# Kernel tuning notes

Measured on AMD Instinct MI355X. Metric: run time of the kernel, lower is better.

Reference implementation:

```python
import jax, jax.numpy as jnp
import numpy as np

N = 100000          # nodes
E = 1600000         # edges (avg degree 16)
F_IN = 128          # node_feature_dim
D = 64              # state_dim
LATENT = 32         # latent_dim -> output 2*latent
ROUNDS = 4


def setup_inputs() -> dict:
    key = jax.random.key(0)
    ks = jax.random.split(key, 12)
    s = 0.05  # weight scale
    return {
        "x": jax.random.normal(ks[0], (N, F_IN), dtype=jnp.float32),
        "edge_index": jax.random.randint(ks[1], (2, E), 0, N, dtype=jnp.int64),
        "batch": jnp.zeros((N,), dtype=jnp.int64),
        # input MLP: Linear(F_IN, D) + ReLU + Linear(D, D) + ReLU
        "W1": jax.random.normal(ks[2], (F_IN, D), dtype=jnp.float32) * s,
        "b1": jnp.zeros((D,), dtype=jnp.float32),
        "W2": jax.random.normal(ks[3], (D, D), dtype=jnp.float32) * s,
        "b2": jnp.zeros((D,), dtype=jnp.float32),
        # per-round GraphConv params (PyG: lin_rel has bias, lin_root does not)
        "Wrel": jax.random.normal(ks[4], (ROUNDS, D, D), dtype=jnp.float32) * s,
        "brel": jnp.zeros((ROUNDS, D), dtype=jnp.float32),
        "Wroot": jax.random.normal(ks[5], (ROUNDS, D, D), dtype=jnp.float32) * s,
        # output Linear(D, 2*latent)
        "Wout": jax.random.normal(ks[6], (D, 2 * LATENT), dtype=jnp.float32) * s,
        "bout": jnp.zeros((2 * LATENT,), dtype=jnp.float32),
    }


def reference(x, edge_index, batch, W1, b1, W2, b2, Wrel, brel, Wroot, Wout, bout):
    # input MLP (ends with ReLU) followed by the extra F.relu in forward (idempotent, kept for fidelity)
    h = jax.nn.relu(x @ W1 + b1)
    h = jax.nn.relu(h @ W2 + b2)
    h = jax.nn.relu(h)
    src, dst = edge_index[0], edge_index[1]
    n = h.shape[0]
    num_rounds = Wrel.shape[0]
    for r in range(num_rounds):
        # GraphConv: scatter-add of source features to destinations, then lin_rel + lin_root
        agg = jax.ops.segment_sum(h[src], dst, num_segments=n)  # [N, D]
        conv = agg @ Wrel[r] + brel[r] + h @ Wroot[r]
        h = h + jax.nn.relu(conv)  # residual
    return h @ Wout + bout  # [N, 2*latent]
```

## Files before the change

### kernel.cpp

```cpp
#include <hip/hip_runtime.h>
#include <hip/hip_bf16.h>

#define CAP 48
#define NPASS 4
#define WP 72
#define WP1 136

typedef __attribute__((ext_vector_type(8))) _Float16 f16x8;
typedef __attribute__((ext_vector_type(4))) float f32x4;

__global__ void k_init(int4* __restrict__ deg4, _Float16* __restrict__ hh,
                       int ndeg4, int n)
{
    const int i = blockIdx.x * 256 + threadIdx.x;
    const int4 z = {0, 0, 0, 0};
    for (int j = i; j < ndeg4; j += gridDim.x * 256) deg4[j] = z;
    if (blockIdx.x == 0 && threadIdx.x < 64)
        hh[(size_t)n * 64 + threadIdx.x] = (_Float16)0.f;
}

__global__ void k_fillp(const int* __restrict__ ei, int* __restrict__ deg,
                        int* __restrict__ colp, int E, int lo, int hi)
{
    int e = blockIdx.x * 256 + threadIdx.x;
    if (e < E) {
        int dst = ei[E + e];
        if (dst >= lo && dst < hi) {
            int pos = atomicAdd(&deg[dst], 1);
            if (pos < CAP) colp[(size_t)dst * CAP + pos] = ei[e];
        }
    }
}

__global__ void k_pad(const int* __restrict__ deg, int* __restrict__ colp, int n)
{
    const int i = blockIdx.x * 256 + threadIdx.x;
    const int node = i >> 4, s = i & 15;
    if (node < n) {
        const int cnt = min(deg[node], CAP);
        const int end = (cnt + 15) & ~15;
        const int slot = cnt + s;
        if (slot < end) colp[(size_t)node * CAP + slot] = n;
    }
}

__global__ __launch_bounds__(256) void k_gather(
    const _Float16* __restrict__ hh, _Float16* __restrict__ aggh,
    const int* __restrict__ colp, const int* __restrict__ deg, int n)
{
    const int w = threadIdx.x >> 6, lane = threadIdx.x & 63;
    const int r = lane >> 3, c = lane & 7;
    const int node = blockIdx.x * 4 + w;
    if (node >= n) return;
    const int cnt = min(deg[node], CAP);

    const int* cb = &colp[(size_t)node * CAP];
    f16x8 s0 = {}; f16x8 s1 = {};
    for (int jb = 0; jb < cnt; jb += 16) {
        const int2 cq = *(const int2*)&cb[jb + 2 * r];
        s0 += *(const f16x8*)&hh[(size_t)cq.x * 64 + c * 8];
        s1 += *(const f16x8*)&hh[(size_t)cq.y * 64 + c * 8];
    }
    s0 += s1;
    #pragma unroll
    for (int st = 8; st <= 32; st <<= 1) {
        uint4 u = *(uint4*)&s0, t;
        t.x = __shfl_xor(u.x, st);
        t.y = __shfl_xor(u.y, st);
        t.z = __shfl_xor(u.z, st);
        t.w = __shfl_xor(u.w, st);
        s0 += *(f16x8*)&t;
    }
    if (r == 0)
        *(uint4*)&aggh[(size_t)node * 64 + c * 8] = *(uint4*)&s0;
}


__global__ __launch_bounds__(256) void k_mlp_mfma(
    const float* __restrict__ x,
    const float* __restrict__ W1, const float* __restrict__ b1,
    const float* __restrict__ W2, const float* __restrict__ b2,
    _Float16* __restrict__ hh, int n)
{
    __shared__ _Float16 W1T[64 * WP1];
    __shared__ _Float16 W2T[64 * WP];
    __shared__ _Float16 t1[4][16 * WP];
    __shared__ float b1s[64], b2s[64];

    const int tid = threadIdx.x;
    for (int i = tid; i < 128 * 64; i += 256) {
        const int k = i >> 6, c = i & 63;
        W1T[c * WP1 + k] = (_Float16)W1[i];
    }
    for (int i = tid; i < 64 * 64; i += 256) {
        const int k = i >> 6, c = i & 63;
        W2T[c * WP + k] = (_Float16)W2[i];
    }
    if (tid < 64) { b1s[tid] = b1[tid]; b2s[tid] = b2[tid]; }
    __syncthreads();

    const int w = tid >> 6, l = tid & 63;
    const int lr = l & 15, lk = l >> 4;
    const int koff = lk * 8;
    const int ntile = (n + 63) >> 6;
    _Float16* T = t1[w];

    for (int t = blockIdx.x; t < ntile; t += gridDim.x) {
        const int row0 = t * 64 + w * 16;
        const size_t xrow = (size_t)min(row0 + lr, n - 1) * 128;
        f16x8 aX[4];
        #pragma unroll
        for (int kb = 0; kb < 4; ++kb) {
            float xf[8];
            *(float4*)&xf[0] = *(const float4*)&x[xrow + kb * 32 + koff];
            *(float4*)&xf[4] = *(const float4*)&x[xrow + kb * 32 + koff + 4];
            f16x8 r;
            #pragma unroll
            for (int i = 0; i < 8; ++i) r[i] = (_Float16)xf[i];
            aX[kb] = r;
        }
        #pragma unroll
        for (int ni = 0; ni < 4; ++ni) {
            const int c = ni * 16 + lr;
            const float bias = b1s[c];
            f32x4 acc = {bias, bias, bias, bias};
            #pragma unroll
            for (int kb = 0; kb < 4; ++kb) {
                const f16x8 bW = *(const f16x8*)&W1T[c * WP1 + kb * 32 + koff];
                acc = __builtin_amdgcn_mfma_f32_16x16x32_f16(aX[kb], bW, acc, 0, 0, 0);
            }
            #pragma unroll
            for (int r = 0; r < 4; ++r)
                T[(lk * 4 + r) * WP + c] = (_Float16)fmaxf(acc[r], 0.f);
        }
        const f16x8 aH0 = *(const f16x8*)&T[lr * WP + koff];
        const f16x8 aH1 = *(const f16x8*)&T[lr * WP + 32 + koff];
        #pragma unroll
        for (int ni = 0; ni < 4; ++ni) {
            const int c = ni * 16 + lr;
            const float bias = b2s[c];
            f32x4 acc = {bias, bias, bias, bias};
            const f16x8 b0 = *(const f16x8*)&W2T[c * WP + koff];
            const f16x8 b1f = *(const f16x8*)&W2T[c * WP + 32 + koff];
            acc = __builtin_amdgcn_mfma_f32_16x16x32_f16(aH0, b0, acc, 0, 0, 0);
            acc = __builtin_amdgcn_mfma_f32_16x16x32_f16(aH1, b1f, acc, 0, 0, 0);
            #pragma unroll
            for (int r = 0; r < 4; ++r) {
                const int row = row0 + lk * 4 + r;
                if (row < n)
                    hh[(size_t)row * 64 + c] = (_Float16)fmaxf(acc[r], 0.f);
            }
        }
    }
}

template<bool LAST>
__global__ __launch_bounds__(256) void k_round_mfma(
    const _Float16* __restrict__ aggh,
    _Float16* hh,
    const float* __restrict__ Wrel, const float* __restrict__ brel,
    const float* __restrict__ Wroot,
    const float* __restrict__ Wout, const float* __restrict__ bout,
    float* __restrict__ out, int n)
{
    __shared__ _Float16 WrT[64 * WP];
    __shared__ _Float16 WoT[64 * WP];
    __shared__ _Float16 WTl[LAST ? 64 * WP : 4];
    __shared__ _Float16 t1[LAST ? 4 : 1][16 * WP];
    __shared__ float bs[64], bso[64];
    const int tid = threadIdx.x;
    for (int i = tid; i < 4096; i += 256) {
        const int k = i >> 6, c = i & 63;
        WrT[c * WP + k] = (_Float16)Wrel[i];
        WoT[c * WP + k] = (_Float16)Wroot[i];
        if constexpr (LAST) WTl[c * WP + k] = (_Float16)Wout[i];
    }
    if (tid < 64) {
        bs[tid] = brel[tid];
        if constexpr (LAST) bso[tid] = bout[tid];
    }
    __syncthreads();

    const int w = tid >> 6, l = tid & 63;
    const int lr = l & 15, lk = l >> 4;
    const int koff = lk * 8;
    const int ntile = (n + 63) >> 6;
    _Float16* T = t1[LAST ? w : 0];

    for (int t = blockIdx.x; t < ntile; t += gridDim.x) {
        const int row0 = t * 64 + w * 16;
        const size_t mrow = (size_t)min(row0 + lr, n - 1) * 64;
        const f16x8 aA0 = *(const f16x8*)&aggh[mrow + koff];
        const f16x8 aA1 = *(const f16x8*)&aggh[mrow + 32 + koff];
        const f16x8 aH0 = *(const f16x8*)&hh  [mrow + koff];
        const f16x8 aH1 = *(const f16x8*)&hh  [mrow + 32 + koff];
        #pragma unroll
        for (int ni = 0; ni < 4; ++ni) {
            const int c = ni * 16 + lr;
            const float bias = bs[c];
            f32x4 acc = {bias, bias, bias, bias};
            const f16x8 br0 = *(const f16x8*)&WrT[c * WP + koff];
            const f16x8 br1 = *(const f16x8*)&WrT[c * WP + 32 + koff];
            const f16x8 bo0 = *(const f16x8*)&WoT[c * WP + koff];
            const f16x8 bo1 = *(const f16x8*)&WoT[c * WP + 32 + koff];
            acc = __builtin_amdgcn_mfma_f32_16x16x32_f16(aA0, br0, acc, 0, 0, 0);
            acc = __builtin_amdgcn_mfma_f32_16x16x32_f16(aA1, br1, acc, 0, 0, 0);
            acc = __builtin_amdgcn_mfma_f32_16x16x32_f16(aH0, bo0, acc, 0, 0, 0);
            acc = __builtin_amdgcn_mfma_f32_16x16x32_f16(aH1, bo1, acc, 0, 0, 0);
            #pragma unroll
            for (int r = 0; r < 4; ++r) {
                const int row = row0 + lk * 4 + r;
                const size_t idx = (size_t)min(row, n - 1) * 64 + c;
                const float v = (float)hh[idx] + fmaxf(acc[r], 0.f);
                if constexpr (LAST) {
                    T[(lk * 4 + r) * WP + c] = (_Float16)v;
                } else {
                    if (row < n) hh[idx] = (_Float16)v;
                }
            }
        }
        if constexpr (LAST) {
            const f16x8 aV0 = *(const f16x8*)&T[lr * WP + koff];
            const f16x8 aV1 = *(const f16x8*)&T[lr * WP + 32 + koff];
            #pragma unroll
            for (int ni = 0; ni < 4; ++ni) {
                const int c = ni * 16 + lr;
                const float bias = bso[c];
                f32x4 acc = {bias, bias, bias, bias};
                const f16x8 w0 = *(const f16x8*)&WTl[c * WP + koff];
                const f16x8 w1 = *(const f16x8*)&WTl[c * WP + 32 + koff];
                acc = __builtin_amdgcn_mfma_f32_16x16x32_f16(aV0, w0, acc, 0, 0, 0);
                acc = __builtin_amdgcn_mfma_f32_16x16x32_f16(aV1, w1, acc, 0, 0, 0);
                #pragma unroll
                for (int r = 0; r < 4; ++r) {
                    const int row = row0 + lk * 4 + r;
                    if (row < n) out[(size_t)row * 64 + c] = acc[r];
                }
            }
        }
    }
}

extern "C" void kernel_launch(void* const* d_in, const int* in_sizes, int n_in,
                              void* d_out, int out_size, void* d_ws, size_t ws_size,
                              hipStream_t stream)
{
    const float* x    = (const float*)d_in[0];
    const int*   ei   = (const int*)  d_in[1];
    const float* W1   = (const float*)d_in[3];
    const float* b1   = (const float*)d_in[4];
    const float* W2   = (const float*)d_in[5];
    const float* b2   = (const float*)d_in[6];
    const float* Wrel = (const float*)d_in[7];
    const float* brel = (const float*)d_in[8];
    const float* Wroot= (const float*)d_in[9];
    const float* Wout = (const float*)d_in[10];
    const float* bout = (const float*)d_in[11];

    const int n = in_sizes[0] / 128;
    const int E = in_sizes[1] / 2;
    const int R = in_sizes[7] / (64 * 64);

    char* p = (char*)d_ws;
    _Float16* hh   = (_Float16*)p; p += (size_t)(n + 1) * 64 * sizeof(_Float16);
    _Float16* aggh = (_Float16*)p; p += (size_t)n * 64 * sizeof(_Float16);
    int*      deg  = (int*)p;      p += (size_t)(n + 4) * sizeof(int);
    int*      colp = (int*)p;      p += (size_t)n * CAP * sizeof(int);
    (void)ws_size; (void)n_in; (void)out_size;

    const int ebl = (E + 255) / 256;

    k_init<<<256, 256, 0, stream>>>((int4*)deg, hh, (n + 3) / 4, n);
    for (int ps = 0; ps < NPASS; ++ps) {
        const int lo = (int)((long)n * ps / NPASS);
        const int hi = (int)((long)n * (ps + 1) / NPASS);
        k_fillp<<<ebl, 256, 0, stream>>>(ei, deg, colp, E, lo, hi);
    }
    k_pad<<<(n * 16 + 255) / 256, 256, 0, stream>>>(deg, colp, n);

    k_mlp_mfma<<<1024, 256, 0, stream>>>(x, W1, b1, W2, b2, hh, n);

    for (int r = 0; r < R; ++r) {
        k_gather<<<(n + 3) / 4, 256, 0, stream>>>(hh, aggh, colp, deg, n);
        const float* Wr = Wrel + (size_t)r * 64 * 64;
        const float* br = brel + (size_t)r * 64;
        const float* Wo = Wroot + (size_t)r * 64 * 64;
        if (r == R - 1)
            k_round_mfma<true><<<1024, 256, 0, stream>>>(
                aggh, hh, Wr, br, Wo, Wout, bout, (float*)d_out, n);
        else
            k_round_mfma<false><<<1024, 256, 0, stream>>>(
                aggh, hh, Wr, br, Wo, Wout, bout, (float*)d_out, n);
    }
}
```

Before: 335.3 us.

## Fuse neighbor gather into per-round MFMA kernel with ping-pong feature buffers

```diff
diff --git a/kernel.cpp b/kernel.cpp
--- a/kernel.cpp
+++ b/kernel.cpp
@@ -9,14 +9,16 @@
 typedef __attribute__((ext_vector_type(8))) _Float16 f16x8;
 typedef __attribute__((ext_vector_type(4))) float f32x4;
 
-__global__ void k_init(int4* __restrict__ deg4, _Float16* __restrict__ hh,
-                       int ndeg4, int n)
+__global__ void k_init(int4* __restrict__ deg4, _Float16* __restrict__ hA,
+                       _Float16* __restrict__ hB, int ndeg4, int n)
 {
     const int i = blockIdx.x * 256 + threadIdx.x;
     const int4 z = {0, 0, 0, 0};
     for (int j = i; j < ndeg4; j += gridDim.x * 256) deg4[j] = z;
-    if (blockIdx.x == 0 && threadIdx.x < 64)
-        hh[(size_t)n * 64 + threadIdx.x] = (_Float16)0.f;
+    if (blockIdx.x == 0 && threadIdx.x < 64) {
+        hA[(size_t)n * 64 + threadIdx.x] = (_Float16)0.f;
+        hB[(size_t)n * 64 + threadIdx.x] = (_Float16)0.f;
+    }
 }
 
 __global__ void k_fillp(const int* __restrict__ ei, int* __restrict__ deg,
@@ -42,37 +44,6 @@
         const int slot = cnt + s;
         if (slot < end) colp[(size_t)node * CAP + slot] = n;
     }
-}
-
-__global__ __launch_bounds__(256) void k_gather(
-    const _Float16* __restrict__ hh, _Float16* __restrict__ aggh,
-    const int* __restrict__ colp, const int* __restrict__ deg, int n)
-{
-    const int w = threadIdx.x >> 6, lane = threadIdx.x & 63;
-    const int r = lane >> 3, c = lane & 7;
-    const int node = blockIdx.x * 4 + w;
-    if (node >= n) return;
-    const int cnt = min(deg[node], CAP);
-
-    const int* cb = &colp[(size_t)node * CAP];
-    f16x8 s0 = {}; f16x8 s1 = {};
-    for (int jb = 0; jb < cnt; jb += 16) {
-        const int2 cq = *(const int2*)&cb[jb + 2 * r];
-        s0 += *(const f16x8*)&hh[(size_t)cq.x * 64 + c * 8];
-        s1 += *(const f16x8*)&hh[(size_t)cq.y * 64 + c * 8];
-    }
-    s0 += s1;
-    #pragma unroll
-    for (int st = 8; st <= 32; st <<= 1) {
-        uint4 u = *(uint4*)&s0, t;
-        t.x = __shfl_xor(u.x, st);
-        t.y = __shfl_xor(u.y, st);
-        t.z = __shfl_xor(u.z, st);
-        t.w = __shfl_xor(u.w, st);
-        s0 += *(f16x8*)&t;
-    }
-    if (r == 0)
-        *(uint4*)&aggh[(size_t)node * 64 + c * 8] = *(uint4*)&s0;
 }
 
 
@@ -155,9 +126,9 @@
 }
 
 template<bool LAST>
-__global__ __launch_bounds__(256) void k_round_mfma(
-    const _Float16* __restrict__ aggh,
-    _Float16* hh,
+__global__ __launch_bounds__(256) void k_round_fused(
+    const _Float16* __restrict__ hin, _Float16* __restrict__ hout,
+    const int* __restrict__ colp, const int* __restrict__ deg,
     const float* __restrict__ Wrel, const float* __restrict__ brel,
     const float* __restrict__ Wroot,
     const float* __restrict__ Wout, const float* __restrict__ bout,
@@ -166,7 +137,7 @@
     __shared__ _Float16 WrT[64 * WP];
     __shared__ _Float16 WoT[64 * WP];
     __shared__ _Float16 WTl[LAST ? 64 * WP : 4];
-    __shared__ _Float16 t1[LAST ? 4 : 1][16 * WP];
+    __shared__ _Float16 aggT[4][16 * WP];
     __shared__ float bs[64], bso[64];
     const int tid = threadIdx.x;
     for (int i = tid; i < 4096; i += 256) {
@@ -183,17 +154,43 @@
 
     const int w = tid >> 6, l = tid & 63;
     const int lr = l & 15, lk = l >> 4;
+    const int gr = l >> 3, gc = l & 7;
     const int koff = lk * 8;
     const int ntile = (n + 63) >> 6;
-    _Float16* T = t1[LAST ? w : 0];
+    _Float16* T = aggT[w];
 
     for (int t = blockIdx.x; t < ntile; t += gridDim.x) {
         const int row0 = t * 64 + w * 16;
+
+        for (int i = 0; i < 16; ++i) {
+            const int node = min(row0 + i, n - 1);
+            const int cnt = min(deg[node], CAP);
+            const int* cb = &colp[(size_t)node * CAP];
+            f16x8 s0 = {}; f16x8 s1 = {};
+            for (int jb = 0; jb < cnt; jb += 16) {
+                const int2 cq = *(const int2*)&cb[jb + 2 * gr];
+                s0 += *(const f16x8*)&hin[(size_t)cq.x * 64 + gc * 8];
+                s1 += *(const f16x8*)&hin[(size_t)cq.y * 64 + gc * 8];
+            }
+            s0 += s1;
+            #pragma unroll
+            for (int st = 8; st <= 32; st <<= 1) {
+                uint4 u = *(uint4*)&s0, tt;
+                tt.x = __shfl_xor(u.x, st);
+                tt.y = __shfl_xor(u.y, st);
+                tt.z = __shfl_xor(u.z, st);
+                tt.w = __shfl_xor(u.w, st);
+                s0 += *(f16x8*)&tt;
+            }
+            if (gr == 0)
+                *(uint4*)&T[i * WP + gc * 8] = *(uint4*)&s0;
+        }
+
         const size_t mrow = (size_t)min(row0 + lr, n - 1) * 64;
-        const f16x8 aA0 = *(const f16x8*)&aggh[mrow + koff];
-        const f16x8 aA1 = *(const f16x8*)&aggh[mrow + 32 + koff];
-        const f16x8 aH0 = *(const f16x8*)&hh  [mrow + koff];
-        const f16x8 aH1 = *(const f16x8*)&hh  [mrow + 32 + koff];
+        const f16x8 aA0 = *(const f16x8*)&T[lr * WP + koff];
+        const f16x8 aA1 = *(const f16x8*)&T[lr * WP + 32 + koff];
+        const f16x8 aH0 = *(const f16x8*)&hin[mrow + koff];
+        const f16x8 aH1 = *(const f16x8*)&hin[mrow + 32 + koff];
         #pragma unroll
         for (int ni = 0; ni < 4; ++ni) {
             const int c = ni * 16 + lr;
@@ -211,11 +208,11 @@
             for (int r = 0; r < 4; ++r) {
                 const int row = row0 + lk * 4 + r;
                 const size_t idx = (size_t)min(row, n - 1) * 64 + c;
-                const float v = (float)hh[idx] + fmaxf(acc[r], 0.f);
+                const float v = (float)hin[idx] + fmaxf(acc[r], 0.f);
                 if constexpr (LAST) {
                     T[(lk * 4 + r) * WP + c] = (_Float16)v;
                 } else {
-                    if (row < n) hh[idx] = (_Float16)v;
+                    if (row < n) hout[idx] = (_Float16)v;
                 }
             }
         }
@@ -262,15 +259,16 @@
     const int R = in_sizes[7] / (64 * 64);
 
     char* p = (char*)d_ws;
-    _Float16* hh   = (_Float16*)p; p += (size_t)(n + 1) * 64 * sizeof(_Float16);
-    _Float16* aggh = (_Float16*)p; p += (size_t)n * 64 * sizeof(_Float16);
+    _Float16* hA   = (_Float16*)p; p += (size_t)(n + 1) * 64 * sizeof(_Float16);
+    _Float16* hB   = (_Float16*)p; p += (size_t)(n + 1) * 64 * sizeof(_Float16);
     int*      deg  = (int*)p;      p += (size_t)(n + 4) * sizeof(int);
     int*      colp = (int*)p;      p += (size_t)n * CAP * sizeof(int);
     (void)ws_size; (void)n_in; (void)out_size;
 
-    const int ebl = (E + 255) / 256;
-
-    k_init<<<256, 256, 0, stream>>>((int4*)deg, hh, (n + 3) / 4, n);
+    const int ebl   = (E + 255) / 256;
+    const int ntile = (n + 63) / 64;
+
+    k_init<<<256, 256, 0, stream>>>((int4*)deg, hA, hB, (n + 3) / 4, n);
     for (int ps = 0; ps < NPASS; ++ps) {
         const int lo = (int)((long)n * ps / NPASS);
         const int hi = (int)((long)n * (ps + 1) / NPASS);
@@ -278,18 +276,20 @@
     }
     k_pad<<<(n * 16 + 255) / 256, 256, 0, stream>>>(deg, colp, n);
 
-    k_mlp_mfma<<<1024, 256, 0, stream>>>(x, W1, b1, W2, b2, hh, n);
-
+    k_mlp_mfma<<<1024, 256, 0, stream>>>(x, W1, b1, W2, b2, hA, n);
+
+    const _Float16* hin = hA;
+    _Float16*       ho  = hB;
     for (int r = 0; r < R; ++r) {
-        k_gather<<<(n + 3) / 4, 256, 0, stream>>>(hh, aggh, colp, deg, n);
         const float* Wr = Wrel + (size_t)r * 64 * 64;
         const float* br = brel + (size_t)r * 64;
         const float* Wo = Wroot + (size_t)r * 64 * 64;
         if (r == R - 1)
-            k_round_mfma<true><<<1024, 256, 0, stream>>>(
-                aggh, hh, Wr, br, Wo, Wout, bout, (float*)d_out, n);
+            k_round_fused<true><<<ntile, 256, 0, stream>>>(
+                hin, ho, colp, deg, Wr, br, Wo, Wout, bout, (float*)d_out, n);
         else
-            k_round_mfma<false><<<1024, 256, 0, stream>>>(
-                aggh, hh, Wr, br, Wo, Wout, bout, (float*)d_out, n);
-    }
-}
+            k_round_fused<false><<<ntile, 256, 0, stream>>>(
+                hin, ho, colp, deg, Wr, br, Wo, Wout, bout, (float*)d_out, n);
+        const _Float16* tswap = hin; hin = ho; ho = (_Float16*)tswap;
+    }
+}
```

Result: slower. 499.2 us (+48.9%).

## Merge CSR build kernels into one cooperative kernel and mask gather tail

Applied to the files above, without the earlier changes.

```diff
diff --git a/kernel.cpp b/kernel.cpp
--- a/kernel.cpp
+++ b/kernel.cpp
@@ -1,5 +1,8 @@
 #include <hip/hip_runtime.h>
 #include <hip/hip_bf16.h>
+#include <hip/hip_cooperative_groups.h>
+
+namespace cg = cooperative_groups;
 
 #define CAP 48
 #define NPASS 4
@@ -9,38 +12,29 @@
 typedef __attribute__((ext_vector_type(8))) _Float16 f16x8;
 typedef __attribute__((ext_vector_type(4))) float f32x4;
 
-__global__ void k_init(int4* __restrict__ deg4, _Float16* __restrict__ hh,
-                       int ndeg4, int n)
-{
-    const int i = blockIdx.x * 256 + threadIdx.x;
-    const int4 z = {0, 0, 0, 0};
-    for (int j = i; j < ndeg4; j += gridDim.x * 256) deg4[j] = z;
-    if (blockIdx.x == 0 && threadIdx.x < 64)
-        hh[(size_t)n * 64 + threadIdx.x] = (_Float16)0.f;
-}
-
-__global__ void k_fillp(const int* __restrict__ ei, int* __restrict__ deg,
-                        int* __restrict__ colp, int E, int lo, int hi)
-{
-    int e = blockIdx.x * 256 + threadIdx.x;
-    if (e < E) {
-        int dst = ei[E + e];
-        if (dst >= lo && dst < hi) {
-            int pos = atomicAdd(&deg[dst], 1);
-            if (pos < CAP) colp[(size_t)dst * CAP + pos] = ei[e];
-        }
-    }
-}
-
-__global__ void k_pad(const int* __restrict__ deg, int* __restrict__ colp, int n)
-{
-    const int i = blockIdx.x * 256 + threadIdx.x;
-    const int node = i >> 4, s = i & 15;
-    if (node < n) {
-        const int cnt = min(deg[node], CAP);
-        const int end = (cnt + 15) & ~15;
-        const int slot = cnt + s;
-        if (slot < end) colp[(size_t)node * CAP + slot] = n;
+__global__ __launch_bounds__(256) void k_build(
+    const int* __restrict__ ei, int* __restrict__ deg, int* __restrict__ colp,
+    _Float16* __restrict__ hh, int E, int n)
+{
+    cg::grid_group grid = cg::this_grid();
+    const int gsz = gridDim.x * 256;
+    const int gid = blockIdx.x * 256 + threadIdx.x;
+
+    for (int j = gid; j < n; j += gsz) deg[j] = 0;
+    if (gid < 64) hh[(size_t)n * 64 + gid] = (_Float16)0.f;
+    grid.sync();
+
+    for (int ps = 0; ps < NPASS; ++ps) {
+        const int lo = (int)((long)n * ps / NPASS);
+        const int hi = (int)((long)n * (ps + 1) / NPASS);
+        for (int e = gid; e < E; e += gsz) {
+            const int dst = ei[E + e];
+            if (dst >= lo && dst < hi) {
+                const int pos = atomicAdd(&deg[dst], 1);
+                if (pos < CAP) colp[(size_t)dst * CAP + pos] = ei[e];
+            }
+        }
+        grid.sync();
     }
 }
 
@@ -49,17 +43,26 @@
     const int* __restrict__ colp, const int* __restrict__ deg, int n)
 {
     const int w = threadIdx.x >> 6, lane = threadIdx.x & 63;
-    const int r = lane >> 3, c = lane & 7;
+    const int gr = lane >> 3, gc = lane & 7;
     const int node = blockIdx.x * 4 + w;
     if (node >= n) return;
     const int cnt = min(deg[node], CAP);
 
     const int* cb = &colp[(size_t)node * CAP];
     f16x8 s0 = {}; f16x8 s1 = {};
-    for (int jb = 0; jb < cnt; jb += 16) {
-        const int2 cq = *(const int2*)&cb[jb + 2 * r];
-        s0 += *(const f16x8*)&hh[(size_t)cq.x * 64 + c * 8];
-        s1 += *(const f16x8*)&hh[(size_t)cq.y * 64 + c * 8];
+    int jb = 0;
+    for (; jb + 16 <= cnt; jb += 16) {
+        const int2 cq = *(const int2*)&cb[jb + 2 * gr];
+        s0 += *(const f16x8*)&hh[(size_t)cq.x * 64 + gc * 8];
+        s1 += *(const f16x8*)&hh[(size_t)cq.y * 64 + gc * 8];
+    }
+    if (jb < cnt) {
+        const int2 cq = *(const int2*)&cb[jb + 2 * gr];
+        const int e0 = jb + 2 * gr;
+        const int i0 = (e0     < cnt) ? cq.x : n;
+        const int i1 = (e0 + 1 < cnt) ? cq.y : n;
+        s0 += *(const f16x8*)&hh[(size_t)i0 * 64 + gc * 8];
+        s1 += *(const f16x8*)&hh[(size_t)i1 * 64 + gc * 8];
     }
     s0 += s1;
     #pragma unroll
@@ -71,8 +74,8 @@
         t.w = __shfl_xor(u.w, st);
         s0 += *(f16x8*)&t;
     }
-    if (r == 0)
-        *(uint4*)&aggh[(size_t)node * 64 + c * 8] = *(uint4*)&s0;
+    if (gr == 0)
+        *(uint4*)&aggh[(size_t)node * 64 + gc * 8] = *(uint4*)&s0;
 }
 
 
@@ -268,15 +271,13 @@
     int*      colp = (int*)p;      p += (size_t)n * CAP * sizeof(int);
     (void)ws_size; (void)n_in; (void)out_size;
 
-    const int ebl = (E + 255) / 256;
-
-    k_init<<<256, 256, 0, stream>>>((int4*)deg, hh, (n + 3) / 4, n);
-    for (int ps = 0; ps < NPASS; ++ps) {
-        const int lo = (int)((long)n * ps / NPASS);
-        const int hi = (int)((long)n * (ps + 1) / NPASS);
-        k_fillp<<<ebl, 256, 0, stream>>>(ei, deg, colp, E, lo, hi);
-    }
-    k_pad<<<(n * 16 + 255) / 256, 256, 0, stream>>>(deg, colp, n);
+    {
+        int E_ = E, n_ = n;
+        void* args[] = {(void*)&ei, (void*)&deg, (void*)&colp,
+                        (void*)&hh, (void*)&E_, (void*)&n_};
+        hipLaunchCooperativeKernel((void*)k_build, dim3(1024), dim3(256),
+                                   args, 0, stream);
+    }
 
     k_mlp_mfma<<<1024, 256, 0, stream>>>(x, W1, b1, W2, b2, hh, n);
 
```

After: 831.6 us. +148.1%, slower.
